# Kernel tuning notes

Measured on AMD Instinct MI355X. Metric: run time of the kernel, lower is better.

Reference implementation:

```python
import jax, jax.numpy as jnp
import numpy as np

N_FFT = 2048
HOP = 512
SR = 48000
T = 2_880_000  # 60 s stereo @ 48 kHz, multiple of HOP


def _hann(n):
    # torch.hann_window default (periodic=True)
    return (0.5 - 0.5 * jnp.cos(2.0 * jnp.pi * jnp.arange(n) / n)).astype(jnp.float32)


def _stft(x, win):
    # x: [C, T] -> [C, F, bins] complex64 (torch.stft center=True, reflect pad)
    pad = N_FFT // 2
    xp = jnp.pad(x, ((0, 0), (pad, pad)), mode='reflect')
    n_frames = 1 + (xp.shape[-1] - N_FFT) // HOP
    idx = jnp.arange(n_frames)[:, None] * HOP + jnp.arange(N_FFT)[None, :]
    frames = xp[:, idx] * win  # [C, F, N_FFT]
    return jnp.fft.rfft(frames, axis=-1)


def _istft(S, win, length):
    # S: [C, F, bins] -> [C, length]; overlap-add with window-square normalization
    frames = jnp.fft.irfft(S, n=N_FFT, axis=-1) * win  # [C, F, N_FFT]
    nF = frames.shape[1]
    total = (nF - 1) * HOP + N_FFT
    idx = jnp.arange(nF)[:, None] * HOP + jnp.arange(N_FFT)[None, :]
    ola = jnp.zeros((frames.shape[0], total), frames.dtype).at[:, idx].add(frames)
    wsum = jnp.zeros((total,), win.dtype).at[idx].add(jnp.broadcast_to(win ** 2, idx.shape))
    out = ola / jnp.where(wsum > 1e-11, wsum, 1.0)
    pad = N_FFT // 2
    return out[:, pad:pad + length]


def _eq_band(audio, freq, gain_db, q=1.0):
    win = _hann(N_FFT)
    S = _stft(audio, win)  # [C, F, bins]
    bins = S.shape[-1]
    freqs = jnp.linspace(0.0, 24000.0, bins)
    mask = jnp.exp(-((freqs - freq) / (freq / q)) ** 2)  # [bins]
    g_lin = 10.0 ** (gain_db / 20.0)
    S = S * (1.0 + (g_lin - 1.0) * mask)
    return _istft(S, win, audio.shape[-1])


def _compress(audio, threshold, ratio, attack, release, makeup_gain):
    aa = jnp.abs(audio) + 1e-8
    adb = 20.0 * jnp.log10(aa)
    gr = jnp.maximum(adb - threshold, 0.0) * (1.0 - 1.0 / ratio)  # [C, T]
    a_att = 1.0 - jnp.exp(-1.0 / (attack * SR))
    a_rel = 1.0 - jnp.exp(-1.0 / (release * SR))

    def step(prev, g):
        alpha = jnp.where(g > prev, a_att, a_rel)
        new = (1.0 - alpha) * prev + alpha * g
        return new, new

    init = jnp.zeros((audio.shape[0],), audio.dtype)
    _, gs = jax.lax.scan(step, init, gr[:, 1:].T)  # [T-1, C]
    gain_smooth = jnp.concatenate([init[:, None], gs.T], axis=1)  # [C, T]
    gain_lin = 10.0 ** ((-gain_smooth + makeup_gain) / 20.0)
    return jnp.sign(audio) * aa * gain_lin


def setup_inputs() -> dict:
    key = jax.random.key(0)
    audio = 0.1 * jax.random.normal(key, (2, T), dtype=jnp.float32)
    f32 = lambda v: jnp.float32(v)
    return {
        'audio': audio,
        'eq_low_gain': f32(3.0),
        'eq_low_mid_gain': f32(-2.0),
        'eq_high_mid_gain': f32(2.5),
        'eq_high_gain': f32(1.5),
        'comp_threshold': f32(-18.0),
        'comp_ratio': f32(4.0),
        'comp_attack': f32(0.01),
        'comp_release': f32(0.1),
        'comp_makeup_gain': f32(3.0),
        'saturation': f32(1.5),
    }


def reference(audio, eq_low_gain, eq_low_mid_gain, eq_high_mid_gain, eq_high_gain,
              comp_threshold, comp_ratio, comp_attack, comp_release,
              comp_makeup_gain, saturation):
    x = _eq_band(audio, 100.0, eq_low_gain)
    x = _eq_band(x, 500.0, eq_low_mid_gain)
    x = _eq_band(x, 3000.0, eq_high_mid_gain)
    x = _eq_band(x, 10000.0, eq_high_gain)
    x = _compress(x, comp_threshold, comp_ratio, comp_attack, comp_release, comp_makeup_gain)
    # saturation branch (original: python if on .item(); here jnp.where)
    return jnp.where(saturation > 1.0, jnp.tanh(x * saturation) / saturation, x)
```

## Files before the change

### kernel.cpp

```cpp
#include <hip/hip_runtime.h>
#include <math.h>

#define T_LEN   2880000
#define LASTFR  5625
#define NBLK_EQ 625
#define SEG     7680
#define NSEG    375
#define KREC    15
#define NREC    512
#define PROWS   528
#define RST     384
#define PL      (PROWS * RST)
#define SPL     (NREC * RST)

typedef float2 c2;
__device__ __forceinline__ c2 cadd(c2 a, c2 b){ return make_float2(a.x+b.x, a.y+b.y); }
__device__ __forceinline__ c2 csub(c2 a, c2 b){ return make_float2(a.x-b.x, a.y-b.y); }
__device__ __forceinline__ c2 cmul(c2 a, c2 b){ return make_float2(a.x*b.x - a.y*b.y, a.x*b.y + a.y*b.x); }
__device__ __forceinline__ c2 cmulj(c2 a, c2 b){ return make_float2(a.x*b.x + a.y*b.y, a.y*b.x - a.x*b.y); }

template<int SGN>
__device__ __forceinline__ void dft8(c2 v[8]) {
    const float r = 0.70710678118654752f;
    c2 t0 = cadd(v[0], v[4]), t1 = csub(v[0], v[4]);
    c2 t2 = cadd(v[2], v[6]), t3 = csub(v[2], v[6]);
    c2 u0 = cadd(v[1], v[5]), u1 = csub(v[1], v[5]);
    c2 u2 = cadd(v[3], v[7]), u3 = csub(v[3], v[7]);
    c2 t3r = (SGN < 0) ? make_float2(t3.y, -t3.x) : make_float2(-t3.y, t3.x);
    c2 u3r = (SGN < 0) ? make_float2(u3.y, -u3.x) : make_float2(-u3.y, u3.x);
    c2 E0 = cadd(t0, t2), E2 = csub(t0, t2);
    c2 E1 = cadd(t1, t3r), E3 = csub(t1, t3r);
    c2 O0 = cadd(u0, u2), O2 = csub(u0, u2);
    c2 O1 = cadd(u1, u3r), O3 = csub(u1, u3r);
    c2 O1w = (SGN < 0) ? make_float2(r*(O1.x+O1.y), r*(O1.y-O1.x))
                       : make_float2(r*(O1.x-O1.y), r*(O1.x+O1.y));
    c2 O2w = (SGN < 0) ? make_float2(O2.y, -O2.x) : make_float2(-O2.y, O2.x);
    c2 O3w = (SGN < 0) ? make_float2(r*(O3.y-O3.x), -r*(O3.x+O3.y))
                       : make_float2(-r*(O3.x+O3.y), r*(O3.x-O3.y));
    v[0] = cadd(E0, O0);  v[4] = csub(E0, O0);
    v[1] = cadd(E1, O1w); v[5] = csub(E1, O1w);
    v[2] = cadd(E2, O2w); v[6] = csub(E2, O2w);
    v[3] = cadd(E3, O3w); v[7] = csub(E3, O3w);
}

__device__ __forceinline__ c2 shx(c2 v, int m) {
    return make_float2(__shfl_xor(v.x, m), __shfl_xor(v.y, m));
}

__device__ __forceinline__ void emit_chunk(float* __restrict__ dst, const float* __restrict__ WN,
                                           int cchunk, int tid, c2 r0, c2 r1) {
    const bool edge = (cchunk <= 2) || (cchunk >= 5626);
    #pragma unroll
    for (int q = 0; q < 2; ++q) {
        c2 rr = (q == 0) ? r0 : r1;
        int m = cchunk * 512 + (q << 8) + tid;
        float inv = 0.66666666666667f;
        if (edge) {
            int tmn = (m >= 2048) ? (((m - 2048) >> 9) + 1) : 0;
            int tmx = min(LASTFR, m >> 9);
            float wsum = 0.0f;
            for (int tt = tmn; tt <= tmx; ++tt) {
                float w = WN[m - (tt << 9)];
                wsum += w * w;
            }
            inv = (wsum > 1e-11f) ? (1.0f / wsum) : 1.0f;
        }
        int o = m - 1024;
        dst[o]         = rr.x * inv;
        dst[T_LEN + o] = rr.y * inv;
    }
}

__global__ __launch_bounds__(256) void eq_band_kernel(
    const float* __restrict__ src, float* __restrict__ dst,
    const float* __restrict__ gain_db_p, const float f0)
{
    __shared__ c2 SA[2048];
    __shared__ c2 TWs2[256];
    __shared__ c2 TWs3[32];
    __shared__ float WN[2048];

    const int tid = threadIdx.x;
    const int b   = blockIdx.x;

    const float gdb   = *gain_db_p;
    const float g_lin = exp2f(gdb * 0.16609640474436813f);
    const float gm1   = g_lin - 1.0f;

    const float st2048 = 6.283185307179586f / 2048.0f;
    for (int idx = tid; idx < 2048; idx += 256) {
        WN[idx] = 0.5f - 0.5f * cosf(st2048 * (float)idx);
    }
    {
        int m = tid >> 5, j2 = tid & 31;
        float ang = (6.283185307179586f / 256.0f) * (float)(j2 * m);
        TWs2[tid] = make_float2(cosf(ang), -sinf(ang));
    }
    if (tid < 32) {
        int m = tid >> 2, j = tid & 3;
        float ang = (6.283185307179586f / 32.0f) * (float)(j * m);
        TWs3[tid] = make_float2(cosf(ang), -sinf(ang));
    }

    float wn[8];
    #pragma unroll
    for (int k = 0; k < 8; ++k)
        wn[k] = 0.5f - 0.5f * cosf(st2048 * (float)(tid + (k << 8)));
    c2 tw1[8];
    float mk[8];
    tw1[0] = make_float2(1.0f, 0.0f);
    #pragma unroll
    for (int m = 1; m < 8; ++m) {
        float ang = st2048 * (float)(tid * m);
        tw1[m] = make_float2(cosf(ang), -sinf(ang));
    }
    #pragma unroll
    for (int m = 0; m < 8; ++m) {
        int tt = tid;
        int bb = tt >> 2, jj = tt & 3;
        int qrev = ((jj & 1) << 1) | (jj >> 1);
        int k = (bb >> 3) + ((bb & 7) << 3) + (m << 6) + (qrev << 9);
        int kk = (k > 1024) ? (2048 - k) : k;
        float f = (float)kk * (24000.0f / 1024.0f);
        float d = (f - f0) / f0;
        mk[m] = (1.0f + gm1 * expf(-d * d)) * (1.0f / 2048.0f);
    }
    __syncthreads();

    const int t0   = max(0, 9 * b - 1);
    const int t1   = min(LASTFR, 9 * b + 10);
    const int cmin = 9 * b + 2;
    const int cmax = 9 * b + 10;

    c2 ring[8];
    #pragma unroll
    for (int q = 0; q < 8; ++q) ring[q] = make_float2(0.0f, 0.0f);

    for (int t = t0; t <= t1; ++t) {
        c2 v[8];

        #pragma unroll
        for (int k = 0; k < 8; ++k) {
            int j = tid + (k << 8);
            int ss = t * 512 + j - 1024;
            ss = (ss < 0) ? -ss : ss;
            ss = (ss >= T_LEN) ? (2 * T_LEN - 2 - ss) : ss;
            float w = wn[k];
            v[k] = make_float2(src[ss] * w, src[T_LEN + ss] * w);
        }
        dft8<-1>(v);
        #pragma unroll
        for (int m = 1; m < 8; ++m) v[m] = cmul(v[m], tw1[m]);
        #pragma unroll
        for (int m = 0; m < 8; ++m) SA[tid + (m << 8)] = v[m];
        __syncthreads();

        {
            int c = tid >> 5, j2 = tid & 31;
            int base = (c << 8) + j2;
            #pragma unroll
            for (int k = 0; k < 8; ++k) v[k] = SA[base + (k << 5)];
            dft8<-1>(v);
            #pragma unroll
            for (int m = 1; m < 8; ++m) v[m] = cmul(v[m], TWs2[(m << 5) + j2]);
            __syncthreads();
            #pragma unroll
            for (int m = 0; m < 8; ++m) SA[(c << 8) + (m << 5) + (j2 ^ (m << 2))] = v[m];
        }
        __syncthreads();

        {
            int bb = tid >> 2, j = tid & 3;
            int base = bb << 5, bx = (bb & 7) << 2;
            #pragma unroll
            for (int k = 0; k < 8; ++k) v[k] = SA[base + ((k << 2) ^ bx) + j];
            dft8<-1>(v);
            #pragma unroll
            for (int m = 1; m < 8; ++m) v[m] = cmul(v[m], TWs3[(m << 2) + j]);
            #pragma unroll
            for (int m = 0; m < 8; ++m) {
                c2 w = v[m];
                c2 p = shx(w, 2);
                c2 e  = (j & 2) ? csub(p, w) : cadd(w, p);
                c2 qq = shx(e, 1);
                c2 lo = (j & 1) ? csub(qq, e) : cadd(e, qq);
                c2 hi = (j & 1) ? make_float2(qq.x - e.y, qq.y + e.x)
                                : make_float2(e.x + qq.y, e.y - qq.x);
                w = (j & 2) ? hi : lo;
                float mkv = mk[m];
                w.x *= mkv; w.y *= mkv;
                c2 p2 = shx(w, 1);
                c2 e2 = (j & 1) ? csub(p2, w) : cadd(w, p2);
                c2 q2 = shx(e2, 2);
                c2 lo2 = (j & 1) ? make_float2(e2.x - q2.y, e2.y + q2.x)
                                 : cadd(e2, q2);
                c2 hi2 = (j & 1) ? make_float2(q2.x + e2.y, q2.y - e2.x)
                                 : csub(q2, e2);
                v[m] = (j & 2) ? hi2 : lo2;
            }
            #pragma unroll
            for (int m = 1; m < 8; ++m) v[m] = cmulj(v[m], TWs3[(m << 2) + j]);
            dft8<+1>(v);
            __syncthreads();
            #pragma unroll
            for (int k = 0; k < 8; ++k) SA[base + ((k << 2) ^ bx) + j] = v[k];
        }
        __syncthreads();

        {
            int c = tid >> 5, j2 = tid & 31;
            #pragma unroll
            for (int m = 0; m < 8; ++m) v[m] = SA[(c << 8) + (m << 5) + (j2 ^ (m << 2))];
            #pragma unroll
            for (int m = 1; m < 8; ++m) v[m] = cmulj(v[m], TWs2[(m << 5) + j2]);
            dft8<+1>(v);
            __syncthreads();
            #pragma unroll
            for (int k = 0; k < 8; ++k) SA[(c << 8) + (k << 5) + j2] = v[k];
        }
        __syncthreads();

        {
            #pragma unroll
            for (int m = 0; m < 8; ++m) v[m] = SA[tid + (m << 8)];
            #pragma unroll
            for (int m = 1; m < 8; ++m) v[m] = cmulj(v[m], tw1[m]);
            dft8<+1>(v);
            #pragma unroll
            for (int k = 0; k < 8; ++k) {
                ring[k].x += v[k].x * wn[k];
                ring[k].y += v[k].y * wn[k];
            }
        }
        __syncthreads();

        if (t >= cmin) emit_chunk(dst, WN, t, tid, ring[0], ring[1]);
        #pragma unroll
        for (int q = 0; q < 6; ++q) ring[q] = ring[q + 2];
        ring[6] = make_float2(0.0f, 0.0f);
        ring[7] = make_float2(0.0f, 0.0f);
    }
    for (int c = t1 + 1; c <= cmax; ++c) {
        emit_chunk(dst, WN, c, tid, ring[0], ring[1]);
        #pragma unroll
        for (int q = 0; q < 6; ++q) ring[q] = ring[q + 2];
        ring[6] = make_float2(0.0f, 0.0f);
        ring[7] = make_float2(0.0f, 0.0f);
    }
}

__device__ __forceinline__ float gaval(float v, float thr, float coef) {
    float aa = fabsf(v) + 1e-8f;
    return fmaxf(6.020599913279624f * __log2f(aa) - thr, 0.0f) * coef;
}

__global__ __launch_bounds__(256) void rec15_kernel(
    const float* __restrict__ y, float4* __restrict__ rec,
    const float* __restrict__ thr_p, const float* __restrict__ ratio_p,
    const float* __restrict__ att_p, const float* __restrict__ rel_p)
{
    __shared__ float4 Lsub[32][9][4];
    const int r0 = blockIdx.x * 32;
    const int s0 = blockIdx.y * 64;
    const int c  = blockIdx.z;
    const int tid = threadIdx.x;

    float thr = *thr_p, ratio = *ratio_p;
    float A  = expf(-1.0f / ((*att_p) * 48000.0f));
    float Bc = expf(-1.0f / ((*rel_p) * 48000.0f));
    float ra = (1.0f - Bc) / (1.0f - A);
    float coef = (1.0f - 1.0f / ratio) * (1.0f - A);

    const int rr = tid & 31, cg = tid >> 5;
    const int orow = tid >> 3, oc8 = tid & 7;

    #pragma unroll 1
    for (int it = 0; it < 8; ++it) {
        int s = s0 + it * 8 + cg;
        if (s < NSEG) {
            int r = r0 + rr;
            int li = s * SEG + KREC * r;
            const float* yp = y + (long)c * T_LEN + li;
            float I[16];
            float a = gaval(yp[0], thr, coef);
            if (li == 0) a = 0.0f;
            I[0] = a; I[1] = ra * a;
            #pragma unroll
            for (int n = 1; n < KREC; ++n) {
                a = gaval(yp[n], thr, coef);
                float b = ra * a;
                I[n + 1] = fmaf(Bc, I[n], b);
                #pragma unroll
                for (int j = n; j >= 1; --j)
                    I[j] = fmaxf(fmaf(A, I[j], a), fmaf(Bc, I[j - 1], b));
                I[0] = fmaf(A, I[0], a);
            }
            Lsub[rr][cg][0] = make_float4(I[0],  I[1],  I[2],  I[3]);
            Lsub[rr][cg][1] = make_float4(I[4],  I[5],  I[6],  I[7]);
            Lsub[rr][cg][2] = make_float4(I[8],  I[9],  I[10], I[11]);
            Lsub[rr][cg][3] = make_float4(I[12], I[13], I[14], I[15]);
        }
        __syncthreads();
        int so = s0 + it * 8 + oc8;
        if (so < NSEG) {
            #pragma unroll
            for (int q = 0; q < 4; ++q)
                rec[(long)(c * 4 + q) * PL + (r0 + orow) * RST + 4 + so]
                    = Lsub[orow][oc8][q];
        }
        __syncthreads();
    }
}


struct Rec { float4 a, b, c, d; };

__device__ __forceinline__ void load8(Rec (&bb)[8],
    const float4* p0, const float4* p1, const float4* p2, const float4* p3, int r)
{
    #pragma unroll
    for (int k = 0; k < 8; ++k) {
        int o = (r + k) * RST;
        bb[k].a = p0[o]; bb[k].b = p1[o]; bb[k].c = p2[o]; bb[k].d = p3[o];
    }
}

template<bool STORE>
__device__ __forceinline__ void consume8(Rec (&bb)[8], float* sp, int r, float& p,
                                         const float (&S)[16])
{
    #pragma unroll
    for (int k = 0; k < 8; ++k) {
        Rec v = bb[k];
        float m0 = fmaxf(fmaf(S[0],  p, v.a.x), fmaf(S[1],  p, v.a.y));
        float m1 = fmaxf(fmaf(S[2],  p, v.a.z), fmaf(S[3],  p, v.a.w));
        float m2 = fmaxf(fmaf(S[4],  p, v.b.x), fmaf(S[5],  p, v.b.y));
        float m3 = fmaxf(fmaf(S[6],  p, v.b.z), fmaf(S[7],  p, v.b.w));
        float m4 = fmaxf(fmaf(S[8],  p, v.c.x), fmaf(S[9],  p, v.c.y));
        float m5 = fmaxf(fmaf(S[10], p, v.c.z), fmaf(S[11], p, v.c.w));
        float m6 = fmaxf(fmaf(S[12], p, v.d.x), fmaf(S[13], p, v.d.y));
        float m7 = fmaxf(fmaf(S[14], p, v.d.z), fmaf(S[15], p, v.d.w));
        m0 = fmaxf(m0, m1); m2 = fmaxf(m2, m3);
        m4 = fmaxf(m4, m5); m6 = fmaxf(m6, m7);
        m0 = fmaxf(m0, m2); m4 = fmaxf(m4, m6);
        p = fmaxf(m0, m4);
        if (STORE) sp[(r + k) * RST] = p;
    }
}

template<bool STORE>
__device__ void scan_pass(const float4* p0, const float4* p1, const float4* p2,
                          const float4* p3, float* sp, float& p, const float (&S)[16])
{
    Rec bA[8], bB[8];
    load8(bA, p0, p1, p2, p3, 0);
    __builtin_amdgcn_sched_barrier(0);
    int r = 0;
    #pragma unroll 1
    for (int gg = 0; gg < NREC / 16; ++gg) {
        load8(bB, p0, p1, p2, p3, r + 8);
        __builtin_amdgcn_sched_barrier(0);
        consume8<STORE>(bA, sp, r, p, S);
        __builtin_amdgcn_sched_barrier(0);
        load8(bA, p0, p1, p2, p3, r + 16);
        __builtin_amdgcn_sched_barrier(0);
        consume8<STORE>(bB, sp, r + 8, p, S);
        __builtin_amdgcn_sched_barrier(0);
        r += 16;
    }
}

template<int MODE>
__global__ __launch_bounds__(64, 1) void scan_iter_kernel(
    const float4* __restrict__ rec, float* __restrict__ gsP,
    const float* __restrict__ eIn, float* __restrict__ eOut,
    const float* __restrict__ att_p, const float* __restrict__ rel_p)
{
    int gid = blockIdx.x * 64 + threadIdx.x;
    int g2 = min(gid, 2 * NSEG - 1);
    int c = g2 / NSEG;
    int s = g2 - c * NSEG;

    float A  = expf(-1.0f / ((*att_p) * 48000.0f));
    float Bc = expf(-1.0f / ((*rel_p) * 48000.0f));
    float S[16];
    {
        float pa = 1.0f;
        #pragma unroll
        for (int j = 15; j >= 0; --j) { S[j] = pa; pa *= A; }
        float pb = 1.0f;
        #pragma unroll
        for (int j = 0; j < 16; ++j) { S[j] *= pb; pb *= Bc; }
    }

    float p = 0.0f;
    if (MODE != 0) p = (s == 0) ? 0.0f : eIn[c * NSEG + s - 1];

    const float4* p0 = rec + (long)(c * 4 + 0) * PL + 4 + s;
    const float4* p1 = rec + (long)(c * 4 + 1) * PL + 4 + s;
    const float4* p2 = rec + (long)(c * 4 + 2) * PL + 4 + s;
    const float4* p3 = rec + (long)(c * 4 + 3) * PL + 4 + s;

    if (MODE == 2) {
        float* sbase = gsP + (long)c * SPL + 4 + s;
        scan_pass<true>(p0, p1, p2, p3, sbase, p, S);
    } else {
        scan_pass<false>(p0, p1, p2, p3, nullptr, p, S);
        eOut[c * NSEG + s] = p;
    }
}

__global__ __launch_bounds__(256) void final_kernel(
    const float* __restrict__ y, const float* __restrict__ gsP, float* __restrict__ out,
    const float* __restrict__ thr_p, const float* __restrict__ ratio_p,
    const float* __restrict__ att_p, const float* __restrict__ rel_p,
    const float* __restrict__ mk_p, const float* __restrict__ sat_p)
{
    __shared__ float LP[64][34];
    const int r0 = blockIdx.x * 32;
    const int s0 = blockIdx.y * 64;
    const int c  = blockIdx.z;
    const int tid = threadIdx.x;

    float thr = *thr_p, ratio = *ratio_p, mk = *mk_p, sat = *sat_p;
    float A  = expf(-1.0f / ((*att_p) * 48000.0f));
    float Bc = expf(-1.0f / ((*rel_p) * 48000.0f));
    float ra = (1.0f - Bc) / (1.0f - A);
    float coef = (1.0f - 1.0f / ratio) * (1.0f - A);
    const float* gb = gsP + (long)c * SPL;

    for (int idx = tid; idx < 33 * 64; idx += 256) {
        int rr = idx >> 6, ss = idx & 63;
        int s = s0 + ss;
        float v = 0.0f;
        if (s < NSEG) {
            int row = r0 - 1 + rr;
            if (row >= 0)      v = gb[row * RST + 4 + s];
            else if (s > 0)    v = gb[(NREC - 1) * RST + 4 + s - 1];
        }
        LP[ss][rr] = v;
    }
    __syncthreads();

    #pragma unroll 1
    for (int it = 0; it < 8; ++it) {
        int idx = it * 256 + tid;
        int ss = idx >> 5, rr = idx & 31;
        int s = s0 + ss;
        if (s >= NSEG) continue;
        int r = r0 + rr;
        int li = s * SEG + KREC * r;
        const float* yp = y + (long)c * T_LEN + li;
        float* op = out + (long)c * T_LEN + li;
        float p = LP[ss][rr];
        #pragma unroll
        for (int q = 0; q < KREC; ++q) {
            float v = yp[q];
            float a = gaval(v, thr, coef);
            if (li + q == 0) a = 0.0f;
            p = fmaxf(fmaf(A, p, a), fmaf(Bc, p, ra * a));
            float aa = fabsf(v) + 1e-8f;
            float gl = exp2f((mk - p) * 0.16609640474436813f);
            float ro = aa * gl;
            ro = (v < 0.0f) ? -ro : ro;
            if (sat > 1.0f) ro = tanhf(ro * sat) / sat;
            op[q] = ro;
        }
    }
}

extern "C" void kernel_launch(void* const* d_in, const int* in_sizes, int n_in,
                              void* d_out, int out_size, void* d_ws, size_t ws_size,
                              hipStream_t stream)
{
    const float* audio = (const float*)d_in[0];
    const float* g1    = (const float*)d_in[1];
    const float* g2    = (const float*)d_in[2];
    const float* g3    = (const float*)d_in[3];
    const float* g4    = (const float*)d_in[4];
    const float* thr   = (const float*)d_in[5];
    const float* ratio = (const float*)d_in[6];
    const float* att   = (const float*)d_in[7];
    const float* rel   = (const float*)d_in[8];
    const float* mkup  = (const float*)d_in[9];
    const float* sat   = (const float*)d_in[10];

    float* out  = (float*)d_out;
    float* bufA = (float*)d_ws;
    float4* rec = (float4*)(bufA + 2 * T_LEN);
    float*  gsP = (float*)(rec + 8 * (long)PL);
    float*  eA  = gsP + 2 * (long)SPL;
    float*  eB  = eA + 2 * NSEG;

    eq_band_kernel<<<NBLK_EQ, 256, 0, stream>>>(audio, out,  g1, 100.0f);
    eq_band_kernel<<<NBLK_EQ, 256, 0, stream>>>(out,   bufA, g2, 500.0f);
    eq_band_kernel<<<NBLK_EQ, 256, 0, stream>>>(bufA,  out,  g3, 3000.0f);
    eq_band_kernel<<<NBLK_EQ, 256, 0, stream>>>(out,   bufA, g4, 10000.0f);

    dim3 tgrid(NREC / 32, (NSEG + 63) / 64, 2);
    rec15_kernel<<<tgrid, 256, 0, stream>>>(bufA, rec, thr, ratio, att, rel);

    scan_iter_kernel<0><<<12, 64, 0, stream>>>(rec, gsP, nullptr, eA, att, rel);
    scan_iter_kernel<1><<<12, 64, 0, stream>>>(rec, gsP, eA, eB, att, rel);
    scan_iter_kernel<1><<<12, 64, 0, stream>>>(rec, gsP, eB, eA, att, rel);
    scan_iter_kernel<1><<<12, 64, 0, stream>>>(rec, gsP, eA, eB, att, rel);
    scan_iter_kernel<2><<<12, 64, 0, stream>>>(rec, gsP, eB, nullptr, att, rel);

    final_kernel<<<tgrid, 256, 0, stream>>>(bufA, gsP, out,
                                            thr, ratio, att, rel, mkup, sat);
}
```

Measured before the change: 728.7 us.

## Process two STFT frames per iteration with double shared-memory buffers

Restructures the EQ band kernel loop to push two consecutive frames through the FFT, mask and IFFT stages together, each frame in its own shared buffer. Every barrier is now shared by two frames, which halves the number of __syncthreads per frame and gives more independent work between barriers to hide latency. In exchange it doubles the FFT scratch shared memory and raises register pressure from holding two 8-element complex vectors, which may lower occupancy.

Result: slower. 767.4 us (+5.3%).

```diff
diff --git a/kernel.cpp b/kernel.cpp
--- a/kernel.cpp
+++ b/kernel.cpp
@@ -71,11 +71,105 @@
     }
 }
 
+__device__ __forceinline__ void f1_compute(c2 (&v)[8], const float* __restrict__ src,
+        int t, const float (&wn)[8], const c2 (&tw1)[8], int tid) {
+    #pragma unroll
+    for (int k = 0; k < 8; ++k) {
+        int j = tid + (k << 8);
+        int ss = t * 512 + j - 1024;
+        ss = (ss < 0) ? -ss : ss;
+        ss = (ss >= T_LEN) ? (2 * T_LEN - 2 - ss) : ss;
+        float w = wn[k];
+        v[k] = make_float2(src[ss] * w, src[T_LEN + ss] * w);
+    }
+    dft8<-1>(v);
+    #pragma unroll
+    for (int m = 1; m < 8; ++m) v[m] = cmul(v[m], tw1[m]);
+}
+__device__ __forceinline__ void sa_store_lin(const c2 (&v)[8], c2* SA, int tid) {
+    #pragma unroll
+    for (int m = 0; m < 8; ++m) SA[tid + (m << 8)] = v[m];
+}
+__device__ __forceinline__ void f2_compute(c2 (&v)[8], const c2* SA, const c2* TWs2, int tid) {
+    int c = tid >> 5, j2 = tid & 31;
+    int base = (c << 8) + j2;
+    #pragma unroll
+    for (int k = 0; k < 8; ++k) v[k] = SA[base + (k << 5)];
+    dft8<-1>(v);
+    #pragma unroll
+    for (int m = 1; m < 8; ++m) v[m] = cmul(v[m], TWs2[(m << 5) + j2]);
+}
+__device__ __forceinline__ void f2_store(const c2 (&v)[8], c2* SA, int tid) {
+    int c = tid >> 5, j2 = tid & 31;
+    #pragma unroll
+    for (int m = 0; m < 8; ++m) SA[(c << 8) + (m << 5) + (j2 ^ (m << 2))] = v[m];
+}
+__device__ __forceinline__ void f3_compute(c2 (&v)[8], const c2* SA, const c2* TWs3,
+                                           const float (&mk)[8], int tid) {
+    int bb = tid >> 2, j = tid & 3;
+    int base = bb << 5, bx = (bb & 7) << 2;
+    #pragma unroll
+    for (int k = 0; k < 8; ++k) v[k] = SA[base + ((k << 2) ^ bx) + j];
+    dft8<-1>(v);
+    #pragma unroll
+    for (int m = 1; m < 8; ++m) v[m] = cmul(v[m], TWs3[(m << 2) + j]);
+    #pragma unroll
+    for (int m = 0; m < 8; ++m) {
+        c2 w = v[m];
+        c2 p = shx(w, 2);
+        c2 e  = (j & 2) ? csub(p, w) : cadd(w, p);
+        c2 qq = shx(e, 1);
+        c2 lo = (j & 1) ? csub(qq, e) : cadd(e, qq);
+        c2 hi = (j & 1) ? make_float2(qq.x - e.y, qq.y + e.x)
+                        : make_float2(e.x + qq.y, e.y - qq.x);
+        w = (j & 2) ? hi : lo;
+        float mkv = mk[m];
+        w.x *= mkv; w.y *= mkv;
+        c2 p2 = shx(w, 1);
+        c2 e2 = (j & 1) ? csub(p2, w) : cadd(w, p2);
+        c2 q2 = shx(e2, 2);
+        c2 lo2 = (j & 1) ? make_float2(e2.x - q2.y, e2.y + q2.x)
+                         : cadd(e2, q2);
+        c2 hi2 = (j & 1) ? make_float2(q2.x + e2.y, q2.y - e2.x)
+                         : csub(q2, e2);
+        v[m] = (j & 2) ? hi2 : lo2;
+    }
+    #pragma unroll
+    for (int m = 1; m < 8; ++m) v[m] = cmulj(v[m], TWs3[(m << 2) + j]);
+    dft8<+1>(v);
+}
+__device__ __forceinline__ void f3_store(const c2 (&v)[8], c2* SA, int tid) {
+    int bb = tid >> 2, j = tid & 3;
+    int base = bb << 5, bx = (bb & 7) << 2;
+    #pragma unroll
+    for (int k = 0; k < 8; ++k) SA[base + ((k << 2) ^ bx) + j] = v[k];
+}
+__device__ __forceinline__ void i3_compute(c2 (&v)[8], const c2* SA, const c2* TWs2, int tid) {
+    int c = tid >> 5, j2 = tid & 31;
+    #pragma unroll
+    for (int m = 0; m < 8; ++m) v[m] = SA[(c << 8) + (m << 5) + (j2 ^ (m << 2))];
+    #pragma unroll
+    for (int m = 1; m < 8; ++m) v[m] = cmulj(v[m], TWs2[(m << 5) + j2]);
+    dft8<+1>(v);
+}
+__device__ __forceinline__ void i3_store(const c2 (&v)[8], c2* SA, int tid) {
+    int c = tid >> 5, j2 = tid & 31;
+    #pragma unroll
+    for (int k = 0; k < 8; ++k) SA[(c << 8) + (k << 5) + j2] = v[k];
+}
+__device__ __forceinline__ void i4_compute(c2 (&v)[8], const c2* SA, const c2 (&tw1)[8], int tid) {
+    #pragma unroll
+    for (int m = 0; m < 8; ++m) v[m] = SA[tid + (m << 8)];
+    #pragma unroll
+    for (int m = 1; m < 8; ++m) v[m] = cmulj(v[m], tw1[m]);
+    dft8<+1>(v);
+}
+
 __global__ __launch_bounds__(256) void eq_band_kernel(
     const float* __restrict__ src, float* __restrict__ dst,
     const float* __restrict__ gain_db_p, const float f0)
 {
-    __shared__ c2 SA[2048];
+    __shared__ c2 SA[2][2048];
     __shared__ c2 TWs2[256];
     __shared__ c2 TWs3[32];
     __shared__ float WN[2048];
@@ -136,104 +230,76 @@
     #pragma unroll
     for (int q = 0; q < 8; ++q) ring[q] = make_float2(0.0f, 0.0f);
 
-    for (int t = t0; t <= t1; ++t) {
+    int t = t0;
+    #pragma unroll 1
+    for (; t + 1 <= t1; t += 2) {
+        c2 vA[8], vB[8];
+        f1_compute(vA, src, t,     wn, tw1, tid);
+        f1_compute(vB, src, t + 1, wn, tw1, tid);
+        sa_store_lin(vA, SA[0], tid); sa_store_lin(vB, SA[1], tid);
+        __syncthreads();
+        f2_compute(vA, SA[0], TWs2, tid); f2_compute(vB, SA[1], TWs2, tid);
+        __syncthreads();
+        f2_store(vA, SA[0], tid); f2_store(vB, SA[1], tid);
+        __syncthreads();
+        f3_compute(vA, SA[0], TWs3, mk, tid); f3_compute(vB, SA[1], TWs3, mk, tid);
+        __syncthreads();
+        f3_store(vA, SA[0], tid); f3_store(vB, SA[1], tid);
+        __syncthreads();
+        i3_compute(vA, SA[0], TWs2, tid); i3_compute(vB, SA[1], TWs2, tid);
+        __syncthreads();
+        i3_store(vA, SA[0], tid); i3_store(vB, SA[1], tid);
+        __syncthreads();
+        i4_compute(vA, SA[0], tw1, tid); i4_compute(vB, SA[1], tw1, tid);
+        __syncthreads();
+
+        #pragma unroll
+        for (int k = 0; k < 8; ++k) {
+            ring[k].x += vA[k].x * wn[k];
+            ring[k].y += vA[k].y * wn[k];
+        }
+        if (t >= cmin) emit_chunk(dst, WN, t, tid, ring[0], ring[1]);
+        #pragma unroll
+        for (int q = 0; q < 6; ++q) ring[q] = ring[q + 2];
+        ring[6] = make_float2(0.0f, 0.0f);
+        ring[7] = make_float2(0.0f, 0.0f);
+
+        #pragma unroll
+        for (int k = 0; k < 8; ++k) {
+            ring[k].x += vB[k].x * wn[k];
+            ring[k].y += vB[k].y * wn[k];
+        }
+        if (t + 1 >= cmin) emit_chunk(dst, WN, t + 1, tid, ring[0], ring[1]);
+        #pragma unroll
+        for (int q = 0; q < 6; ++q) ring[q] = ring[q + 2];
+        ring[6] = make_float2(0.0f, 0.0f);
+        ring[7] = make_float2(0.0f, 0.0f);
+    }
+    #pragma unroll 1
+    for (; t <= t1; ++t) {
         c2 v[8];
-
+        f1_compute(v, src, t, wn, tw1, tid);
+        sa_store_lin(v, SA[0], tid);
+        __syncthreads();
+        f2_compute(v, SA[0], TWs2, tid);
+        __syncthreads();
+        f2_store(v, SA[0], tid);
+        __syncthreads();
+        f3_compute(v, SA[0], TWs3, mk, tid);
+        __syncthreads();
+        f3_store(v, SA[0], tid);
+        __syncthreads();
+        i3_compute(v, SA[0], TWs2, tid);
+        __syncthreads();
+        i3_store(v, SA[0], tid);
+        __syncthreads();
+        i4_compute(v, SA[0], tw1, tid);
+        __syncthreads();
         #pragma unroll
         for (int k = 0; k < 8; ++k) {
-            int j = tid + (k << 8);
-            int ss = t * 512 + j - 1024;
-            ss = (ss < 0) ? -ss : ss;
-            ss = (ss >= T_LEN) ? (2 * T_LEN - 2 - ss) : ss;
-            float w = wn[k];
-            v[k] = make_float2(src[ss] * w, src[T_LEN + ss] * w);
-        }
-        dft8<-1>(v);
-        #pragma unroll
-        for (int m = 1; m < 8; ++m) v[m] = cmul(v[m], tw1[m]);
-        #pragma unroll
-        for (int m = 0; m < 8; ++m) SA[tid + (m << 8)] = v[m];
-        __syncthreads();
-
-        {
-            int c = tid >> 5, j2 = tid & 31;
-            int base = (c << 8) + j2;
-            #pragma unroll
-            for (int k = 0; k < 8; ++k) v[k] = SA[base + (k << 5)];
-            dft8<-1>(v);
-            #pragma unroll
-            for (int m = 1; m < 8; ++m) v[m] = cmul(v[m], TWs2[(m << 5) + j2]);
-            __syncthreads();
-            #pragma unroll
-            for (int m = 0; m < 8; ++m) SA[(c << 8) + (m << 5) + (j2 ^ (m << 2))] = v[m];
-        }
-        __syncthreads();
-
-        {
-            int bb = tid >> 2, j = tid & 3;
-            int base = bb << 5, bx = (bb & 7) << 2;
-            #pragma unroll
-            for (int k = 0; k < 8; ++k) v[k] = SA[base + ((k << 2) ^ bx) + j];
-            dft8<-1>(v);
-            #pragma unroll
-            for (int m = 1; m < 8; ++m) v[m] = cmul(v[m], TWs3[(m << 2) + j]);
-            #pragma unroll
-            for (int m = 0; m < 8; ++m) {
-                c2 w = v[m];
-                c2 p = shx(w, 2);
-                c2 e  = (j & 2) ? csub(p, w) : cadd(w, p);
-                c2 qq = shx(e, 1);
-                c2 lo = (j & 1) ? csub(qq, e) : cadd(e, qq);
-                c2 hi = (j & 1) ? make_float2(qq.x - e.y, qq.y + e.x)
-                                : make_float2(e.x + qq.y, e.y - qq.x);
-                w = (j & 2) ? hi : lo;
-                float mkv = mk[m];
-                w.x *= mkv; w.y *= mkv;
-                c2 p2 = shx(w, 1);
-                c2 e2 = (j & 1) ? csub(p2, w) : cadd(w, p2);
-                c2 q2 = shx(e2, 2);
-                c2 lo2 = (j & 1) ? make_float2(e2.x - q2.y, e2.y + q2.x)
-                                 : cadd(e2, q2);
-                c2 hi2 = (j & 1) ? make_float2(q2.x + e2.y, q2.y - e2.x)
-                                 : csub(q2, e2);
-                v[m] = (j & 2) ? hi2 : lo2;
-            }
-            #pragma unroll
-            for (int m = 1; m < 8; ++m) v[m] = cmulj(v[m], TWs3[(m << 2) + j]);
-            dft8<+1>(v);
-            __syncthreads();
-            #pragma unroll
-            for (int k = 0; k < 8; ++k) SA[base + ((k << 2) ^ bx) + j] = v[k];
-        }
-        __syncthreads();
-
-        {
-            int c = tid >> 5, j2 = tid & 31;
-            #pragma unroll
-            for (int m = 0; m < 8; ++m) v[m] = SA[(c << 8) + (m << 5) + (j2 ^ (m << 2))];
-            #pragma unroll
-            for (int m = 1; m < 8; ++m) v[m] = cmulj(v[m], TWs2[(m << 5) + j2]);
-            dft8<+1>(v);
-            __syncthreads();
-            #pragma unroll
-            for (int k = 0; k < 8; ++k) SA[(c << 8) + (k << 5) + j2] = v[k];
-        }
-        __syncthreads();
-
-        {
-            #pragma unroll
-            for (int m = 0; m < 8; ++m) v[m] = SA[tid + (m << 8)];
-            #pragma unroll
-            for (int m = 1; m < 8; ++m) v[m] = cmulj(v[m], tw1[m]);
-            dft8<+1>(v);
-            #pragma unroll
-            for (int k = 0; k < 8; ++k) {
-                ring[k].x += v[k].x * wn[k];
-                ring[k].y += v[k].y * wn[k];
-            }
-        }
-        __syncthreads();
-
+            ring[k].x += v[k].x * wn[k];
+            ring[k].y += v[k].y * wn[k];
+        }
         if (t >= cmin) emit_chunk(dst, WN, t, tid, ring[0], ring[1]);
         #pragma unroll
         for (int q = 0; q < 6; ++q) ring[q] = ring[q + 2];
```
